# Performance work log

Hardware: AMD Instinct MI355X
Metric: run time of the kernel (lower is better)

Reference implementation:

```python
import jax, jax.numpy as jnp
import numpy as np

L, D, H, G, HS, I, V, B, T = 4, 1024, 16, 4, 64, 2816, 32000, 4, 512
THETA = 10000.0
EPS = 1e-6


def setup_inputs() -> dict:
    key = jax.random.key(0)
    ks = jax.random.split(key, 10)
    s = 0.02
    return {
        "input_ids": jax.random.randint(ks[0], (B, T), 0, V),
        "embed": jax.random.normal(ks[1], (V, D)) * s,      # tied with lm_head
        "q_w": jax.random.normal(ks[2], (L, D, D)) * s,     # torch Linear: [out, in]
        "q_b": jax.random.normal(ks[3], (L, D)) * s,
        "kv_w": jax.random.normal(ks[4], (L, 2 * G * HS, D)) * s,
        "kv_b": jax.random.normal(ks[5], (L, 2 * G * HS)) * s,
        "o_w": jax.random.normal(ks[6], (L, D, D)) * s,
        "ln1_w": jnp.ones((L, D)),
        "ln2_w": jnp.ones((L, D)),
        "gate_w": jax.random.normal(ks[7], (L, I, D)) * s,
        "up_w": jax.random.normal(ks[8], (L, I, D)) * s,
        "down_w": jax.random.normal(ks[9], (L, D, I)) * s,
        "last_w": jnp.ones((D,)),
    }


def rms_norm(x, w):
    return x * jax.lax.rsqrt(jnp.mean(x * x, axis=-1, keepdims=True) + EPS) * w


def rope_tables(t, hs):
    inv_freq = 1.0 / (THETA ** (jnp.arange(0, hs, 2, dtype=jnp.float32) / hs))
    ang = jnp.arange(t, dtype=jnp.float32)[:, None] * inv_freq[None, :]  # [T, hs/2]
    emb = jnp.concatenate([ang, ang], axis=-1)                           # [T, hs]
    return jnp.cos(emb), jnp.sin(emb)


def rotate_half(x):
    x1, x2 = jnp.split(x, 2, axis=-1)
    return jnp.concatenate([-x2, x1], axis=-1)


def reference(input_ids, embed, q_w, q_b, kv_w, kv_b, o_w, ln1_w, ln2_w, gate_w, up_w, down_w, last_w):
    x = embed[input_ids]  # [B, T, D]
    cos, sin = rope_tables(T, HS)                    # [T, HS] (buffers, const)
    c, s_ = cos[None, None], sin[None, None]         # [1, 1, T, HS]
    causal = jnp.tril(jnp.ones((T, T), dtype=bool))
    scale = 1.0 / np.sqrt(HS).astype(np.float32)
    for l in range(L):
        h = rms_norm(x, ln1_w[l])
        q = (h @ q_w[l].T + q_b[l]).reshape(B, T, H, HS).transpose(0, 2, 1, 3)  # bhtd
        kv = h @ kv_w[l].T + kv_b[l]
        k, v = jnp.split(kv, 2, axis=-1)
        k = k.reshape(B, T, G, HS).transpose(0, 2, 1, 3)  # bgtd
        v = v.reshape(B, T, G, HS).transpose(0, 2, 1, 3)
        k = jnp.repeat(k, H // G, axis=1)  # GQA kv repeat -> bhtd
        v = jnp.repeat(v, H // G, axis=1)
        q = q * c + rotate_half(q) * s_
        k = k * c + rotate_half(k) * s_
        attn = jnp.einsum('bhtd,bhsd->bhts', q, k) * scale
        attn = jnp.where(causal, attn, -jnp.inf)
        attn = jax.nn.softmax(attn, axis=-1)
        o = jnp.einsum('bhts,bhsd->bhtd', attn, v).transpose(0, 2, 1, 3).reshape(B, T, D)
        x = x + o @ o_w[l].T  # o_proj has no bias
        h = rms_norm(x, ln2_w[l])
        x = x + (jax.nn.silu(h @ gate_w[l].T) * (h @ up_w[l].T)) @ down_w[l].T  # SwiGLU
    x = rms_norm(x, last_w)
    return x @ embed.T  # tied lm_head -> logits [B, T, V]
```

## Files before the change

### kernel.cpp

```cpp
#include <hip/hip_runtime.h>
#include <hip/hip_bf16.h>
#include <stdint.h>


typedef __bf16 bf16x8 __attribute__((ext_vector_type(8)));
typedef __bf16 bf16x4 __attribute__((ext_vector_type(4)));
typedef float  f32x4  __attribute__((ext_vector_type(4)));

#define AS1 __attribute__((address_space(1)))
#define AS3 __attribute__((address_space(3)))

__device__ __forceinline__ void gld_lds16(const void* g, void* l) {
  __builtin_amdgcn_global_load_lds((const AS1 void*)g, (AS3 void*)l, 16, 0, 0);
}

__global__ __launch_bounds__(256) void cvt_kernel(const float* __restrict__ in,
                                                  __bf16* __restrict__ out, int n4) {
  for (int i = blockIdx.x * 256 + threadIdx.x; i < n4; i += gridDim.x * 256) {
    f32x4 v = __builtin_nontemporal_load(&((const f32x4*)in)[i]);
    bf16x4 o;
#pragma unroll
    for (int j = 0; j < 4; ++j) o[j] = (__bf16)v[j];
    ((bf16x4*)out)[i] = o;
  }
}

__global__ __launch_bounds__(256) void embed_kernel(const int* __restrict__ ids,
                                                    const float* __restrict__ emb,
                                                    float* __restrict__ x) {
  const int tok = blockIdx.x;
  const float* src = emb + (size_t)ids[tok] * 1024;
  float* dst = x + (size_t)tok * 1024;
#pragma unroll
  for (int j = 0; j < 4; ++j) {
    const int d = threadIdx.x + j * 256;
    dst[d] = src[d];
  }
}

__global__ __launch_bounds__(256) void rmsnorm_kernel(const float* __restrict__ x,
                                                      const float* __restrict__ wgt,
                                                      __bf16* __restrict__ out) {
  const int row = blockIdx.x;
  const float* xr = x + (size_t)row * 1024;
  float v[4];
  float ss = 0.f;
#pragma unroll
  for (int j = 0; j < 4; ++j) { v[j] = xr[threadIdx.x + j * 256]; ss += v[j] * v[j]; }
#pragma unroll
  for (int m = 1; m < 64; m <<= 1) ss += __shfl_xor(ss, m, 64);
  __shared__ float red[4];
  if ((threadIdx.x & 63) == 0) red[threadIdx.x >> 6] = ss;
  __syncthreads();
  const float tot = red[0] + red[1] + red[2] + red[3];
  const float sc = rsqrtf(tot * (1.f / 1024.f) + 1e-6f);
#pragma unroll
  for (int j = 0; j < 4; ++j) {
    const int d = threadIdx.x + j * 256;
    out[(size_t)row * 1024 + d] = (__bf16)(v[j] * sc * wgt[d]);
  }
}

#define GEMM_PREAMBLE                                              \
  const int t = threadIdx.x;                                       \
  const int lane = t & 63;                                         \
  const int w = t >> 6, wr = w >> 1, wc = w & 1;                   \
  const int lr = lane & 15;                                        \
  const int lk = (lane >> 4) * 8;                                  \
  const int sr = t >> 2;                                           \
  const int scol = (t & 3) * 8;

#define FLAT_SWZ(BMC, BNC)                                         \
  const int chunk_ = (int)(gridDim.x >> 3);                        \
  const int wg_ = (blockIdx.x & 7) * chunk_ + (blockIdx.x >> 3);   \
  const int bm = wg_ % (BMC);                                      \
  const int rest_ = wg_ / (BMC);                                   \
  const int bn = rest_ % (BNC);                                    \
  const int ks = rest_ / (BNC);                                    \
  (void)ks;

#define GEMM_FRAGS_MFMA                                            \
  bf16x8 af[4], bfr[4];                                            \
  _Pragma("unroll") for (int m = 0; m < 4; ++m)                    \
    af[m] = *(const bf16x8*)&As[(wr * 64 + m * 16 + lr) * 32 + lk];\
  _Pragma("unroll") for (int n = 0; n < 4; ++n)                    \
    bfr[n] = *(const bf16x8*)&Bs[(wc * 64 + n * 16 + lr) * 32 + lk];\
  _Pragma("unroll") for (int m = 0; m < 4; ++m)                    \
    _Pragma("unroll") for (int n = 0; n < 4; ++n)                  \
      acc[m][n] = __builtin_amdgcn_mfma_f32_16x16x32_bf16(af[m], bfr[n], acc[m][n], 0, 0, 0);

template <int EPI, int BMC, int BNC, int KSP>
__global__ __launch_bounds__(256) void gemm_bt(const __bf16* __restrict__ A,
                                               const __bf16* __restrict__ Bb,
                                               float* __restrict__ Cf,
                                               int K, int ldc) {
  __shared__ __bf16 As[128 * 32];
  __shared__ __bf16 Bs[128 * 32];
  GEMM_PREAMBLE
  FLAT_SWZ(BMC, BNC)
  const int klen = K / KSP;
  const int kbeg = ks * klen;

  const __bf16* a0 = A + (size_t)(bm * 128 + sr) * K + scol;
  const __bf16* a1 = A + (size_t)(bm * 128 + 64 + sr) * K + scol;
  const __bf16* bb0 = Bb + (size_t)(bn * 128 + sr) * K + scol;
  const __bf16* bb1 = Bb + (size_t)(bn * 128 + 64 + sr) * K + scol;

  f32x4 acc[4][4] = {};
  for (int k0 = kbeg; k0 < kbeg + klen; k0 += 32) {
    gld_lds16(a0 + k0, &As[t * 8]);
    gld_lds16(a1 + k0, &As[2048 + t * 8]);
    gld_lds16(bb0 + k0, &Bs[t * 8]);
    gld_lds16(bb1 + k0, &Bs[2048 + t * 8]);
    __syncthreads();
    GEMM_FRAGS_MFMA
    __syncthreads();
  }
  const int r0 = bm * 128 + wr * 64 + (lane >> 4) * 4;
  const int c0 = bn * 128 + wc * 64 + lr;
#pragma unroll
  for (int m = 0; m < 4; ++m)
#pragma unroll
    for (int r = 0; r < 4; ++r) {
      const size_t rowoff = (size_t)(r0 + m * 16 + r) * ldc;
#pragma unroll
      for (int n = 0; n < 4; ++n) {
        if (EPI == 3) Cf[rowoff + c0 + n * 16] = acc[m][n][r];
        else          atomicAdd(&Cf[rowoff + c0 + n * 16], acc[m][n][r]);
      }
    }
}

__global__ __launch_bounds__(256) void qkv_gemm(const __bf16* __restrict__ A,
                                                const __bf16* __restrict__ qw,
                                                const __bf16* __restrict__ kvw,
                                                const float* __restrict__ q_b,
                                                const float* __restrict__ kv_b,
                                                __bf16* __restrict__ qb,
                                                __bf16* __restrict__ kvb) {
  const int K = 1024;
  __shared__ __bf16 As[128 * 32];
  __shared__ __bf16 Bs[128 * 32];
  GEMM_PREAMBLE
  FLAT_SWZ(16, 12)
  const bool isq = bn < 8;
  const int bnn = isq ? bn : bn - 8;
  const __bf16* Bw = (isq ? qw : kvw) + (size_t)(bnn * 128) * K;

  const __bf16* a0 = A + (size_t)(bm * 128 + sr) * K + scol;
  const __bf16* a1 = A + (size_t)(bm * 128 + 64 + sr) * K + scol;
  const __bf16* bb0 = Bw + (size_t)sr * K + scol;
  const __bf16* bb1 = Bw + (size_t)(64 + sr) * K + scol;

  f32x4 acc[4][4] = {};
  for (int k0 = 0; k0 < K; k0 += 32) {
    gld_lds16(a0 + k0, &As[t * 8]);
    gld_lds16(a1 + k0, &As[2048 + t * 8]);
    gld_lds16(bb0 + k0, &Bs[t * 8]);
    gld_lds16(bb1 + k0, &Bs[2048 + t * 8]);
    __syncthreads();
    GEMM_FRAGS_MFMA
    __syncthreads();
  }

  const int ldc = isq ? 1024 : 512;
  __bf16* out = isq ? qb : kvb;
  const float* bias = isq ? q_b : kv_b;
  const int cb = bnn * 128 + wc * 64;
  const bool dorope = isq || (cb < 256);
  float bv[4];
#pragma unroll
  for (int n = 0; n < 4; ++n) bv[n] = bias[cb + n * 16 + lr];
  float inv0 = __expf((float)lr * -0.28782313662425574f);
  float inv1 = __expf((float)(16 + lr) * -0.28782313662425574f);

  const int r0 = bm * 128 + wr * 64 + (lane >> 4) * 4;
#pragma unroll
  for (int m = 0; m < 4; ++m)
#pragma unroll
    for (int r = 0; r < 4; ++r) {
      const int row = r0 + m * 16 + r;
      float c4[4];
#pragma unroll
      for (int n = 0; n < 4; ++n) c4[n] = acc[m][n][r] + bv[n];
      if (dorope) {
        const float pos = (float)(row & 511);
        float sg, cg;
        __sincosf(pos * inv0, &sg, &cg);
        float x1 = c4[0], x2 = c4[2];
        c4[0] = x1 * cg - x2 * sg;
        c4[2] = x2 * cg + x1 * sg;
        __sincosf(pos * inv1, &sg, &cg);
        x1 = c4[1]; x2 = c4[3];
        c4[1] = x1 * cg - x2 * sg;
        c4[3] = x2 * cg + x1 * sg;
      }
      const size_t rowoff = (size_t)row * ldc;
#pragma unroll
      for (int n = 0; n < 4; ++n) out[rowoff + cb + n * 16 + lr] = (__bf16)c4[n];
    }
}

__global__ __launch_bounds__(256) void gateup_gemm(const __bf16* __restrict__ A,
                                                   const __bf16* __restrict__ gw,
                                                   const __bf16* __restrict__ uw,
                                                   __bf16* __restrict__ gbuf,
                                                   __bf16* __restrict__ ubuf) {
  const int K = 1024;
  __shared__ __bf16 As[128 * 32];
  __shared__ __bf16 Bs[128 * 32];
  GEMM_PREAMBLE
  FLAT_SWZ(16, 44)
  const bool isg = bn < 22;
  const int bnn = isg ? bn : bn - 22;
  const __bf16* Bw = (isg ? gw : uw) + (size_t)(bnn * 128) * K;
  __bf16* out = isg ? gbuf : ubuf;

  const __bf16* a0 = A + (size_t)(bm * 128 + sr) * K + scol;
  const __bf16* a1 = A + (size_t)(bm * 128 + 64 + sr) * K + scol;
  const __bf16* bb0 = Bw + (size_t)sr * K + scol;
  const __bf16* bb1 = Bw + (size_t)(64 + sr) * K + scol;

  f32x4 acc[4][4] = {};
  for (int k0 = 0; k0 < K; k0 += 32) {
    gld_lds16(a0 + k0, &As[t * 8]);
    gld_lds16(a1 + k0, &As[2048 + t * 8]);
    gld_lds16(bb0 + k0, &Bs[t * 8]);
    gld_lds16(bb1 + k0, &Bs[2048 + t * 8]);
    __syncthreads();
    GEMM_FRAGS_MFMA
    __syncthreads();
  }
  const int r0 = bm * 128 + wr * 64 + (lane >> 4) * 4;
  const int c0 = bnn * 128 + wc * 64 + lr;
#pragma unroll
  for (int m = 0; m < 4; ++m)
#pragma unroll
    for (int r = 0; r < 4; ++r) {
      const size_t rowoff = (size_t)(r0 + m * 16 + r) * 2816;
#pragma unroll
      for (int n = 0; n < 4; ++n) out[rowoff + c0 + n * 16] = (__bf16)acc[m][n][r];
    }
}

__global__ __launch_bounds__(256) void down_gemm(const __bf16* __restrict__ g,
                                                 const __bf16* __restrict__ u,
                                                 const __bf16* __restrict__ Bb,
                                                 float* __restrict__ Cf) {
  const int K = 2816;
  __shared__ __bf16 As[128 * 32];
  __shared__ __bf16 Bs[128 * 32];
  GEMM_PREAMBLE
  FLAT_SWZ(16, 8)
  const int klen = 1408;
  const int kbeg = ks * klen;

  const size_t arow0 = (size_t)(bm * 128 + sr) * K + scol;
  const size_t arow1 = (size_t)(bm * 128 + 64 + sr) * K + scol;
  const __bf16* bb0 = Bb + (size_t)(bn * 128 + sr) * K + scol;
  const __bf16* bb1 = Bb + (size_t)(bn * 128 + 64 + sr) * K + scol;

  f32x4 acc[4][4] = {};
  for (int k0 = kbeg; k0 < kbeg + klen; k0 += 32) {
    {
      bf16x8 gv0 = *(const bf16x8*)(g + arow0 + k0);
      bf16x8 uv0 = *(const bf16x8*)(u + arow0 + k0);
      bf16x8 gv1 = *(const bf16x8*)(g + arow1 + k0);
      bf16x8 uv1 = *(const bf16x8*)(u + arow1 + k0);
      bf16x8 s0, s1;
#pragma unroll
      for (int j = 0; j < 8; ++j) {
        const float gf = (float)gv0[j];
        s0[j] = (__bf16)(gf / (1.f + __expf(-gf)) * (float)uv0[j]);
      }
#pragma unroll
      for (int j = 0; j < 8; ++j) {
        const float gf = (float)gv1[j];
        s1[j] = (__bf16)(gf / (1.f + __expf(-gf)) * (float)uv1[j]);
      }
      *(bf16x8*)&As[t * 8] = s0;
      *(bf16x8*)&As[2048 + t * 8] = s1;
    }
    gld_lds16(bb0 + k0, &Bs[t * 8]);
    gld_lds16(bb1 + k0, &Bs[2048 + t * 8]);
    __syncthreads();
    GEMM_FRAGS_MFMA
    __syncthreads();
  }
  const int r0 = bm * 128 + wr * 64 + (lane >> 4) * 4;
  const int c0 = bn * 128 + wc * 64 + lr;
#pragma unroll
  for (int m = 0; m < 4; ++m)
#pragma unroll
    for (int r = 0; r < 4; ++r) {
      const size_t rowoff = (size_t)(r0 + m * 16 + r) * 1024;
#pragma unroll
      for (int n = 0; n < 4; ++n) atomicAdd(&Cf[rowoff + c0 + n * 16], acc[m][n][r]);
    }
}

__global__ __launch_bounds__(512, 2) void lmhead_gemm(const __bf16* __restrict__ A,
                                                      const __bf16* __restrict__ Bb,
                                                      float* __restrict__ C) {
  __shared__ __bf16 lds[2][4][8192];
  const int t = threadIdx.x;
  const int lane = t & 63;
  const int w = t >> 6;
  const int wr = w >> 2;
  const int wc = w & 3;
  const int lr = lane & 15;
  const int lg = lane >> 4;
  const int sx = (lr & 7) << 4;

  const int wg = (blockIdx.x & 7) * 125 + (blockIdx.x >> 3);
  const int bm = wg & 7;
  const int bn = wg >> 3;

  int srow[2], scol[2];
#pragma unroll
  for (int j = 0; j < 2; ++j) {
    const int q = (t + j * 512) * 16;
    const int row = q >> 7;
    const int p = q ^ ((row & 7) << 4);
    srow[j] = row;
    scol[j] = (p & 127) >> 1;
  }

  auto STAGE = [&](int buf, int kt) {
#pragma unroll
    for (int ht = 0; ht < 4; ++ht) {
      const __bf16* base = (ht < 2)
          ? A + (size_t)(bm * 256 + ht * 128) * 1024
          : Bb + (size_t)(bn * 256 + (ht - 2) * 128) * 1024;
#pragma unroll
      for (int j = 0; j < 2; ++j) {
        gld_lds16(base + (size_t)srow[j] * 1024 + kt * 64 + scol[j],
                  (char*)&lds[buf][ht][0] + (size_t)(t + j * 512) * 16);
      }
    }
  };

  STAGE(0, 0);
  STAGE(1, 1);

  f32x4 acc[8][4] = {};
  for (int kt = 0; kt < 16; ++kt) {
    const int cur = kt & 1;
    if (kt < 15) asm volatile("s_waitcnt vmcnt(8)" ::: "memory");
    else         asm volatile("s_waitcnt vmcnt(0)" ::: "memory");
    __builtin_amdgcn_s_barrier();

    const char* Ab = (const char*)&lds[cur][wr][0];
    const char* Bbs = (const char*)&lds[cur][2 + (wc >> 1)][0];
    const int rB0 = (wc & 1) * 64;
#pragma unroll
    for (int ph = 0; ph < 4; ++ph) {
      const int m0 = (ph >> 1) * 4;
      const int n0 = (ph & 1) * 2;
      bf16x8 af[4][2], bfr[2][2];
#pragma unroll
      for (int mi = 0; mi < 4; ++mi)
#pragma unroll
        for (int ksl = 0; ksl < 2; ++ksl) {
          const int row = (m0 + mi) * 16 + lr;
          af[mi][ksl] = *(const bf16x8*)(Ab + ((row * 128 + ksl * 64 + lg * 16) ^ sx));
        }
#pragma unroll
      for (int ni = 0; ni < 2; ++ni)
#pragma unroll
        for (int ksl = 0; ksl < 2; ++ksl) {
          const int row = rB0 + (n0 + ni) * 16 + lr;
          bfr[ni][ksl] = *(const bf16x8*)(Bbs + ((row * 128 + ksl * 64 + lg * 16) ^ sx));
        }
      __builtin_amdgcn_s_setprio(1);
#pragma unroll
      for (int mi = 0; mi < 4; ++mi)
#pragma unroll
        for (int ni = 0; ni < 2; ++ni)
#pragma unroll
          for (int ksl = 0; ksl < 2; ++ksl)
            acc[m0 + mi][n0 + ni] = __builtin_amdgcn_mfma_f32_16x16x32_bf16(
                af[mi][ksl], bfr[ni][ksl], acc[m0 + mi][n0 + ni], 0, 0, 0);
      __builtin_amdgcn_s_setprio(0);
    }
    asm volatile("s_waitcnt lgkmcnt(0)" ::: "memory");
    __builtin_amdgcn_s_barrier();
    if (kt + 2 < 16) STAGE(cur, kt + 2);
  }

  const int r0 = bm * 256 + wr * 128 + lg * 4;
  const int c0 = bn * 256 + wc * 64 + lr;
#pragma unroll
  for (int m = 0; m < 8; ++m)
#pragma unroll
    for (int r = 0; r < 4; ++r) {
      float* crow = C + (size_t)(r0 + m * 16 + r) * 32000 + c0;
#pragma unroll
      for (int n = 0; n < 4; ++n)
        __builtin_nontemporal_store(acc[m][n][r], crow + n * 16);
    }
}

__global__ __launch_bounds__(256) void attn_kernel(const __bf16* __restrict__ q,
                                                   const __bf16* __restrict__ kv,
                                                   __bf16* __restrict__ o) {
  const int qt = blockIdx.x, hh = blockIdx.y, b = blockIdx.z;
  const int g = hh >> 2;
  const int t = threadIdx.x, lane = t & 63, w = t >> 6;
  const int lr = lane & 15, lg = lane >> 4;

  __shared__ __bf16 Vt[64 * 72];
  __shared__ __bf16 Ps[64 * 72];

  bf16x8 qa[2];
  {
    const size_t qoff = ((size_t)(b * 512 + qt * 64 + w * 16 + lr)) * 1024 + hh * 64;
    qa[0] = *(const bf16x8*)(q + qoff + lg * 8);
    qa[1] = *(const bf16x8*)(q + qoff + 32 + lg * 8);
  }

  f32x4 acc_o[4] = {};
  float mrow[4], lrow[4];
#pragma unroll
  for (int r = 0; r < 4; ++r) { mrow[r] = -1e30f; lrow[r] = 0.f; }

  const int srow = t >> 3;
  const int sdv = (t & 7) * 8;

  for (int kt = 0; kt <= qt; ++kt) {
    const size_t krow = ((size_t)(b * 512 + kt * 64 + srow)) * 512;
    {
      const __bf16* vsrc = kv + krow + 256 + g * 64 + sdv;
      bf16x8 v0 = *(const bf16x8*)vsrc;
      bf16x8 v1 = *(const bf16x8*)(vsrc + 32 * 512);
#pragma unroll
      for (int j = 0; j < 8; ++j) Vt[(sdv + j) * 72 + srow] = v0[j];
#pragma unroll
      for (int j = 0; j < 8; ++j) Vt[(sdv + j) * 72 + srow + 32] = v1[j];
    }
    __syncthreads();

    bf16x8 kb[4][2];
#pragma unroll
    for (int nf = 0; nf < 4; ++nf)
#pragma unroll
      for (int kc = 0; kc < 2; ++kc)
        kb[nf][kc] = *(const bf16x8*)(kv +
            ((size_t)(b * 512 + kt * 64 + nf * 16 + lr)) * 512 + g * 64 + kc * 32 + lg * 8);

    f32x4 s[4] = {};
#pragma unroll
    for (int nf = 0; nf < 4; ++nf)
#pragma unroll
      for (int kc = 0; kc < 2; ++kc)
        s[nf] = __builtin_amdgcn_mfma_f32_16x16x32_bf16(qa[kc], kb[nf][kc], s[nf], 0, 0, 0);

    float pm[4][4], mx[4];
    const int qg = qt * 64 + w * 16 + lg * 4;
    const int kg = kt * 64 + lr;
#pragma unroll
    for (int r = 0; r < 4; ++r) mx[r] = -1e30f;
#pragma unroll
    for (int nf = 0; nf < 4; ++nf)
#pragma unroll
      for (int r = 0; r < 4; ++r) {
        float vv = s[nf][r] * 0.125f;
        vv = (kg + nf * 16 <= qg + r) ? vv : -1e30f;
        pm[nf][r] = vv;
        mx[r] = fmaxf(mx[r], vv);
      }
#pragma unroll
    for (int msk = 1; msk < 16; msk <<= 1)
#pragma unroll
      for (int r = 0; r < 4; ++r) mx[r] = fmaxf(mx[r], __shfl_xor(mx[r], msk, 64));

    float rs[4];
#pragma unroll
    for (int r = 0; r < 4; ++r) {
      const float mn = fmaxf(mrow[r], mx[r]);
      const float f = __expf(mrow[r] - mn);
      mrow[r] = mn;
      lrow[r] *= f;
#pragma unroll
      for (int df = 0; df < 4; ++df) acc_o[df][r] *= f;
      float rsum = 0.f;
#pragma unroll
      for (int nf = 0; nf < 4; ++nf) {
        const float pp = __expf(pm[nf][r] - mn);
        pm[nf][r] = pp;
        rsum += pp;
      }
      rs[r] = rsum;
    }
#pragma unroll
    for (int msk = 1; msk < 16; msk <<= 1)
#pragma unroll
      for (int r = 0; r < 4; ++r) rs[r] += __shfl_xor(rs[r], msk, 64);
#pragma unroll
    for (int r = 0; r < 4; ++r) lrow[r] += rs[r];

#pragma unroll
    for (int nf = 0; nf < 4; ++nf)
#pragma unroll
      for (int r = 0; r < 4; ++r)
        Ps[(w * 16 + lg * 4 + r) * 72 + nf * 16 + lr] = (__bf16)pm[nf][r];

#pragma unroll
    for (int df = 0; df < 4; ++df)
#pragma unroll
      for (int kc = 0; kc < 2; ++kc) {
        bf16x8 pa = *(const bf16x8*)&Ps[(w * 16 + lr) * 72 + kc * 32 + lg * 8];
        bf16x8 vb = *(const bf16x8*)&Vt[(df * 16 + lr) * 72 + kc * 32 + lg * 8];
        acc_o[df] = __builtin_amdgcn_mfma_f32_16x16x32_bf16(pa, vb, acc_o[df], 0, 0, 0);
      }
    __syncthreads();
  }

#pragma unroll
  for (int df = 0; df < 4; ++df)
#pragma unroll
    for (int r = 0; r < 4; ++r) {
      const int trow = qt * 64 + w * 16 + lg * 4 + r;
      o[((size_t)(b * 512 + trow)) * 1024 + hh * 64 + df * 16 + lr] =
          (__bf16)(acc_o[df][r] / lrow[r]);
    }
}

extern "C" void kernel_launch(void* const* d_in, const int* in_sizes, int n_in,
                              void* d_out, int out_size, void* d_ws, size_t ws_size,
                              hipStream_t stream) {
  const int* ids = (const int*)d_in[0];
  const float* emb_f = (const float*)d_in[1];
  const float* qw_f = (const float*)d_in[2];
  const float* q_b = (const float*)d_in[3];
  const float* kvw_f = (const float*)d_in[4];
  const float* kv_b = (const float*)d_in[5];
  const float* ow_f = (const float*)d_in[6];
  const float* ln1 = (const float*)d_in[7];
  const float* ln2 = (const float*)d_in[8];
  const float* gw_f = (const float*)d_in[9];
  const float* uw_f = (const float*)d_in[10];
  const float* dw_f = (const float*)d_in[11];
  const float* lw = (const float*)d_in[12];
  float* out = (float*)d_out;

  char* p = (char*)d_ws;
  float* x = (float*)p;        p += (size_t)2048 * 1024 * 4;
  __bf16* h = (__bf16*)p;      p += (size_t)2048 * 1024 * 2;
  __bf16* qb = (__bf16*)p;     p += (size_t)2048 * 1024 * 2;
  __bf16* kvb = (__bf16*)p;    p += (size_t)2048 * 512 * 2;
  __bf16* ao = (__bf16*)p;     p += (size_t)2048 * 1024 * 2;
  __bf16* gb = (__bf16*)p;     p += (size_t)2048 * 2816 * 2;
  __bf16* ub = (__bf16*)p;     p += (size_t)2048 * 2816 * 2;
  __bf16* emb_b = (__bf16*)p;  p += (size_t)32000 * 1024 * 2;
  __bf16* qw_b = (__bf16*)p;   p += (size_t)4 * 1024 * 1024 * 2;
  __bf16* kvw_b = (__bf16*)p;  p += (size_t)4 * 512 * 1024 * 2;
  __bf16* ow_b = (__bf16*)p;   p += (size_t)4 * 1024 * 1024 * 2;
  __bf16* gw_b = (__bf16*)p;   p += (size_t)4 * 2816 * 1024 * 2;
  __bf16* uw_b = (__bf16*)p;   p += (size_t)4 * 2816 * 1024 * 2;
  __bf16* dw_b = (__bf16*)p;   p += (size_t)4 * 2816 * 1024 * 2;

  cvt_kernel<<<2048, 256, 0, stream>>>(emb_f, emb_b, 32000 * 1024 / 4);
  cvt_kernel<<<1024, 256, 0, stream>>>(qw_f, qw_b, 4 * 1024 * 1024 / 4);
  cvt_kernel<<<1024, 256, 0, stream>>>(kvw_f, kvw_b, 4 * 512 * 1024 / 4);
  cvt_kernel<<<1024, 256, 0, stream>>>(ow_f, ow_b, 4 * 1024 * 1024 / 4);
  cvt_kernel<<<1024, 256, 0, stream>>>(gw_f, gw_b, 4 * 2816 * 1024 / 4);
  cvt_kernel<<<1024, 256, 0, stream>>>(uw_f, uw_b, 4 * 2816 * 1024 / 4);
  cvt_kernel<<<1024, 256, 0, stream>>>(dw_f, dw_b, 4 * 2816 * 1024 / 4);

  embed_kernel<<<2048, 256, 0, stream>>>(ids, emb_f, x);
  for (int l = 0; l < 4; ++l) {
    rmsnorm_kernel<<<2048, 256, 0, stream>>>(x, ln1 + l * 1024, h);
    qkv_gemm<<<192, 256, 0, stream>>>(
        h, qw_b + (size_t)l * 1024 * 1024, kvw_b + (size_t)l * 512 * 1024,
        q_b + l * 1024, kv_b + l * 512, qb, kvb);
    attn_kernel<<<dim3(8, 16, 4), 256, 0, stream>>>(qb, kvb, ao);
    gemm_bt<4, 16, 8, 2><<<256, 256, 0, stream>>>(
        ao, ow_b + (size_t)l * 1024 * 1024, x, 1024, 1024);
    rmsnorm_kernel<<<2048, 256, 0, stream>>>(x, ln2 + l * 1024, h);
    gateup_gemm<<<704, 256, 0, stream>>>(
        h, gw_b + (size_t)l * 2816 * 1024, uw_b + (size_t)l * 2816 * 1024, gb, ub);
    down_gemm<<<256, 256, 0, stream>>>(
        gb, ub, dw_b + (size_t)l * 1024 * 2816, x);
  }
  rmsnorm_kernel<<<2048, 256, 0, stream>>>(x, lw, h);
  lmhead_gemm<<<1000, 512, 0, stream>>>(h, emb_b, out);
}
```

Before: 1.064 ms.

## Generalize 256x256 GEMM with finer-grained pipelining and reuse it for gate/up projection

```diff
diff --git a/kernel.cpp b/kernel.cpp
--- a/kernel.cpp
+++ b/kernel.cpp
@@ -201,50 +201,7 @@
     }
 }
 
-__global__ __launch_bounds__(256) void gateup_gemm(const __bf16* __restrict__ A,
-                                                   const __bf16* __restrict__ gw,
-                                                   const __bf16* __restrict__ uw,
-                                                   __bf16* __restrict__ gbuf,
-                                                   __bf16* __restrict__ ubuf) {
-  const int K = 1024;
-  __shared__ __bf16 As[128 * 32];
-  __shared__ __bf16 Bs[128 * 32];
-  GEMM_PREAMBLE
-  FLAT_SWZ(16, 44)
-  const bool isg = bn < 22;
-  const int bnn = isg ? bn : bn - 22;
-  const __bf16* Bw = (isg ? gw : uw) + (size_t)(bnn * 128) * K;
-  __bf16* out = isg ? gbuf : ubuf;
-
-  const __bf16* a0 = A + (size_t)(bm * 128 + sr) * K + scol;
-  const __bf16* a1 = A + (size_t)(bm * 128 + 64 + sr) * K + scol;
-  const __bf16* bb0 = Bw + (size_t)sr * K + scol;
-  const __bf16* bb1 = Bw + (size_t)(64 + sr) * K + scol;
-
-  f32x4 acc[4][4] = {};
-  for (int k0 = 0; k0 < K; k0 += 32) {
-    gld_lds16(a0 + k0, &As[t * 8]);
-    gld_lds16(a1 + k0, &As[2048 + t * 8]);
-    gld_lds16(bb0 + k0, &Bs[t * 8]);
-    gld_lds16(bb1 + k0, &Bs[2048 + t * 8]);
-    __syncthreads();
-    GEMM_FRAGS_MFMA
-    __syncthreads();
-  }
-  const int r0 = bm * 128 + wr * 64 + (lane >> 4) * 4;
-  const int c0 = bnn * 128 + wc * 64 + lr;
-#pragma unroll
-  for (int m = 0; m < 4; ++m)
-#pragma unroll
-    for (int r = 0; r < 4; ++r) {
-      const size_t rowoff = (size_t)(r0 + m * 16 + r) * 2816;
-#pragma unroll
-      for (int n = 0; n < 4; ++n) out[rowoff + c0 + n * 16] = (__bf16)acc[m][n][r];
-    }
-}
-
-__global__ __launch_bounds__(256) void down_gemm(const __bf16* __restrict__ g,
-                                                 const __bf16* __restrict__ u,
+__global__ __launch_bounds__(256) void down_gemm(const __bf16* __restrict__ gu,
                                                  const __bf16* __restrict__ Bb,
                                                  float* __restrict__ Cf) {
   const int K = 2816;
@@ -255,18 +212,18 @@
   const int klen = 1408;
   const int kbeg = ks * klen;
 
-  const size_t arow0 = (size_t)(bm * 128 + sr) * K + scol;
-  const size_t arow1 = (size_t)(bm * 128 + 64 + sr) * K + scol;
+  const size_t arow0 = (size_t)(bm * 128 + sr) * 5632 + scol;
+  const size_t arow1 = (size_t)(bm * 128 + 64 + sr) * 5632 + scol;
   const __bf16* bb0 = Bb + (size_t)(bn * 128 + sr) * K + scol;
   const __bf16* bb1 = Bb + (size_t)(bn * 128 + 64 + sr) * K + scol;
 
   f32x4 acc[4][4] = {};
   for (int k0 = kbeg; k0 < kbeg + klen; k0 += 32) {
     {
-      bf16x8 gv0 = *(const bf16x8*)(g + arow0 + k0);
-      bf16x8 uv0 = *(const bf16x8*)(u + arow0 + k0);
-      bf16x8 gv1 = *(const bf16x8*)(g + arow1 + k0);
-      bf16x8 uv1 = *(const bf16x8*)(u + arow1 + k0);
+      bf16x8 gv0 = *(const bf16x8*)(gu + arow0 + k0);
+      bf16x8 uv0 = *(const bf16x8*)(gu + arow0 + 2816 + k0);
+      bf16x8 gv1 = *(const bf16x8*)(gu + arow1 + k0);
+      bf16x8 uv1 = *(const bf16x8*)(gu + arow1 + 2816 + k0);
       bf16x8 s0, s1;
 #pragma unroll
       for (int j = 0; j < 8; ++j) {
@@ -299,9 +256,19 @@
     }
 }
 
-__global__ __launch_bounds__(512, 2) void lmhead_gemm(const __bf16* __restrict__ A,
-                                                      const __bf16* __restrict__ Bb,
-                                                      float* __restrict__ C) {
+#define SYNC_MFMA(MH, NH, BR)                                      \
+  __builtin_amdgcn_s_barrier();                                    \
+  asm volatile("s_waitcnt lgkmcnt(0)" ::: "memory");               \
+  __builtin_amdgcn_sched_barrier(0);                               \
+  MFMA16(MH, NH, BR);                                              \
+  __builtin_amdgcn_s_barrier();
+
+template <int EPI>
+__global__ __launch_bounds__(512, 2) void gemm256(const __bf16* __restrict__ A,
+                                                  const __bf16* __restrict__ Bb,
+                                                  float* __restrict__ Cf,
+                                                  __bf16* __restrict__ Cb,
+                                                  int ldc) {
   __shared__ __bf16 lds[2][4][8192];
   const int t = threadIdx.x;
   const int lane = t & 63;
@@ -312,7 +279,8 @@
   const int lg = lane >> 4;
   const int sx = (lr & 7) << 4;
 
-  const int wg = (blockIdx.x & 7) * 125 + (blockIdx.x >> 3);
+  const int chunk = (int)gridDim.x >> 3;
+  const int wg = ((int)blockIdx.x & 7) * chunk + ((int)blockIdx.x >> 3);
   const int bm = wg & 7;
   const int bn = wg >> 3;
 
@@ -326,66 +294,90 @@
     scol[j] = (p & 127) >> 1;
   }
 
-  auto STAGE = [&](int buf, int kt) {
-#pragma unroll
-    for (int ht = 0; ht < 4; ++ht) {
-      const __bf16* base = (ht < 2)
-          ? A + (size_t)(bm * 256 + ht * 128) * 1024
-          : Bb + (size_t)(bn * 256 + (ht - 2) * 128) * 1024;
-#pragma unroll
-      for (int j = 0; j < 2; ++j) {
-        gld_lds16(base + (size_t)srow[j] * 1024 + kt * 64 + scol[j],
-                  (char*)&lds[buf][ht][0] + (size_t)(t + j * 512) * 16);
-      }
-    }
+  auto STAGE1 = [&](int buf, int ht, int kt) {
+    const __bf16* base = (ht < 2) ? A + (size_t)(bm * 256 + ht * 128) * 1024
+                                  : Bb + (size_t)(bn * 256 + (ht - 2) * 128) * 1024;
+#pragma unroll
+    for (int j = 0; j < 2; ++j)
+      gld_lds16(base + (size_t)srow[j] * 1024 + kt * 64 + scol[j],
+                (char*)&lds[buf][ht][0] + (size_t)(t + j * 512) * 16);
   };
 
-  STAGE(0, 0);
-  STAGE(1, 1);
-
+  bf16x8 afr[4][2], b0r[2][2], b1r[2][2];
   f32x4 acc[8][4] = {};
-  for (int kt = 0; kt < 16; ++kt) {
-    const int cur = kt & 1;
-    if (kt < 15) asm volatile("s_waitcnt vmcnt(8)" ::: "memory");
-    else         asm volatile("s_waitcnt vmcnt(0)" ::: "memory");
-    __builtin_amdgcn_s_barrier();
-
-    const char* Ab = (const char*)&lds[cur][wr][0];
-    const char* Bbs = (const char*)&lds[cur][2 + (wc >> 1)][0];
-    const int rB0 = (wc & 1) * 64;
-#pragma unroll
-    for (int ph = 0; ph < 4; ++ph) {
-      const int m0 = (ph >> 1) * 4;
-      const int n0 = (ph & 1) * 2;
-      bf16x8 af[4][2], bfr[2][2];
-#pragma unroll
-      for (int mi = 0; mi < 4; ++mi)
-#pragma unroll
-        for (int ksl = 0; ksl < 2; ++ksl) {
-          const int row = (m0 + mi) * 16 + lr;
-          af[mi][ksl] = *(const bf16x8*)(Ab + ((row * 128 + ksl * 64 + lg * 16) ^ sx));
-        }
+
+  auto LDA = [&](int buf, int mh) {
+    const char* Ab = (const char*)&lds[buf][wr][0];
+#pragma unroll
+    for (int mi = 0; mi < 4; ++mi)
+#pragma unroll
+      for (int ksl = 0; ksl < 2; ++ksl) {
+        const int row = (mh * 4 + mi) * 16 + lr;
+        afr[mi][ksl] = *(const bf16x8*)(Ab + ((row * 128 + ksl * 64 + lg * 16) ^ sx));
+      }
+  };
+  auto LDB = [&](int buf, int nh, bf16x8 (&br)[2][2]) {
+    const char* Bs = (const char*)&lds[buf][2 + (wc >> 1)][0];
+    const int rB0 = (wc & 1) * 64 + nh * 32;
+#pragma unroll
+    for (int ni = 0; ni < 2; ++ni)
+#pragma unroll
+      for (int ksl = 0; ksl < 2; ++ksl) {
+        const int row = rB0 + ni * 16 + lr;
+        br[ni][ksl] = *(const bf16x8*)(Bs + ((row * 128 + ksl * 64 + lg * 16) ^ sx));
+      }
+  };
+  auto MFMA16 = [&](int mh, int nh, bf16x8 (&br)[2][2]) {
+    __builtin_amdgcn_s_setprio(1);
+#pragma unroll
+    for (int mi = 0; mi < 4; ++mi)
 #pragma unroll
       for (int ni = 0; ni < 2; ++ni)
 #pragma unroll
-        for (int ksl = 0; ksl < 2; ++ksl) {
-          const int row = rB0 + (n0 + ni) * 16 + lr;
-          bfr[ni][ksl] = *(const bf16x8*)(Bbs + ((row * 128 + ksl * 64 + lg * 16) ^ sx));
-        }
-      __builtin_amdgcn_s_setprio(1);
-#pragma unroll
-      for (int mi = 0; mi < 4; ++mi)
-#pragma unroll
-        for (int ni = 0; ni < 2; ++ni)
-#pragma unroll
-          for (int ksl = 0; ksl < 2; ++ksl)
-            acc[m0 + mi][n0 + ni] = __builtin_amdgcn_mfma_f32_16x16x32_bf16(
-                af[mi][ksl], bfr[ni][ksl], acc[m0 + mi][n0 + ni], 0, 0, 0);
-      __builtin_amdgcn_s_setprio(0);
-    }
-    asm volatile("s_waitcnt lgkmcnt(0)" ::: "memory");
-    __builtin_amdgcn_s_barrier();
-    if (kt + 2 < 16) STAGE(cur, kt + 2);
+        for (int ksl = 0; ksl < 2; ++ksl)
+          acc[mh * 4 + mi][nh * 2 + ni] = __builtin_amdgcn_mfma_f32_16x16x32_bf16(
+              afr[mi][ksl], br[ni][ksl], acc[mh * 4 + mi][nh * 2 + ni], 0, 0, 0);
+    __builtin_amdgcn_s_setprio(0);
+  };
+
+  STAGE1(0, 2, 0); STAGE1(0, 0, 0); STAGE1(0, 3, 0); STAGE1(0, 1, 0);
+  STAGE1(1, 2, 1); STAGE1(1, 0, 1);
+  asm volatile("s_waitcnt vmcnt(4)" ::: "memory");
+  __builtin_amdgcn_s_barrier();
+
+  for (int j = 0; j < 8; ++j) {
+    const int T1 = 2 * j + 1;
+    const bool pf = (j < 7);
+    LDA(0, 0); LDB(0, 0, b0r);
+    STAGE1(1, 3, T1);
+    SYNC_MFMA(0, 0, b0r)
+    LDB(0, 1, b1r);
+    STAGE1(1, 1, T1);
+    SYNC_MFMA(0, 1, b1r)
+    LDA(0, 1);
+    if (pf) STAGE1(0, 2, T1 + 1);
+    SYNC_MFMA(1, 1, b1r)
+    if (pf) {
+      STAGE1(0, 0, T1 + 1);
+      asm volatile("s_waitcnt vmcnt(4)" ::: "memory");
+    } else {
+      asm volatile("s_waitcnt vmcnt(0)" ::: "memory");
+    }
+    SYNC_MFMA(1, 0, b0r)
+    LDA(1, 0); LDB(1, 0, b0r);
+    if (pf) STAGE1(0, 3, T1 + 1);
+    SYNC_MFMA(0, 0, b0r)
+    LDB(1, 1, b1r);
+    if (pf) STAGE1(0, 1, T1 + 1);
+    SYNC_MFMA(0, 1, b1r)
+    LDA(1, 1);
+    if (pf) STAGE1(1, 2, T1 + 2);
+    SYNC_MFMA(1, 1, b1r)
+    if (pf) {
+      STAGE1(1, 0, T1 + 2);
+      asm volatile("s_waitcnt vmcnt(4)" ::: "memory");
+    }
+    SYNC_MFMA(1, 0, b0r)
   }
 
   const int r0 = bm * 256 + wr * 128 + lg * 4;
@@ -394,10 +386,16 @@
   for (int m = 0; m < 8; ++m)
 #pragma unroll
     for (int r = 0; r < 4; ++r) {
-      float* crow = C + (size_t)(r0 + m * 16 + r) * 32000 + c0;
-#pragma unroll
-      for (int n = 0; n < 4; ++n)
-        __builtin_nontemporal_store(acc[m][n][r], crow + n * 16);
+      if (EPI == 0) {
+        float* crow = Cf + (size_t)(r0 + m * 16 + r) * ldc + c0;
+#pragma unroll
+        for (int n = 0; n < 4; ++n)
+          __builtin_nontemporal_store(acc[m][n][r], crow + n * 16);
+      } else {
+        __bf16* crow = Cb + (size_t)(r0 + m * 16 + r) * ldc + c0;
+#pragma unroll
+        for (int n = 0; n < 4; ++n) crow[n * 16] = (__bf16)acc[m][n][r];
+      }
     }
 }
 
@@ -550,22 +548,25 @@
   __bf16* qb = (__bf16*)p;     p += (size_t)2048 * 1024 * 2;
   __bf16* kvb = (__bf16*)p;    p += (size_t)2048 * 512 * 2;
   __bf16* ao = (__bf16*)p;     p += (size_t)2048 * 1024 * 2;
-  __bf16* gb = (__bf16*)p;     p += (size_t)2048 * 2816 * 2;
-  __bf16* ub = (__bf16*)p;     p += (size_t)2048 * 2816 * 2;
+  __bf16* guB = (__bf16*)p;    p += (size_t)2048 * 5632 * 2;
   __bf16* emb_b = (__bf16*)p;  p += (size_t)32000 * 1024 * 2;
   __bf16* qw_b = (__bf16*)p;   p += (size_t)4 * 1024 * 1024 * 2;
   __bf16* kvw_b = (__bf16*)p;  p += (size_t)4 * 512 * 1024 * 2;
   __bf16* ow_b = (__bf16*)p;   p += (size_t)4 * 1024 * 1024 * 2;
-  __bf16* gw_b = (__bf16*)p;   p += (size_t)4 * 2816 * 1024 * 2;
-  __bf16* uw_b = (__bf16*)p;   p += (size_t)4 * 2816 * 1024 * 2;
+  __bf16* guw_b = (__bf16*)p;  p += (size_t)4 * 5632 * 1024 * 2;
   __bf16* dw_b = (__bf16*)p;   p += (size_t)4 * 2816 * 1024 * 2;
 
   cvt_kernel<<<2048, 256, 0, stream>>>(emb_f, emb_b, 32000 * 1024 / 4);
   cvt_kernel<<<1024, 256, 0, stream>>>(qw_f, qw_b, 4 * 1024 * 1024 / 4);
   cvt_kernel<<<1024, 256, 0, stream>>>(kvw_f, kvw_b, 4 * 512 * 1024 / 4);
   cvt_kernel<<<1024, 256, 0, stream>>>(ow_f, ow_b, 4 * 1024 * 1024 / 4);
-  cvt_kernel<<<1024, 256, 0, stream>>>(gw_f, gw_b, 4 * 2816 * 1024 / 4);
-  cvt_kernel<<<1024, 256, 0, stream>>>(uw_f, uw_b, 4 * 2816 * 1024 / 4);
+  for (int l = 0; l < 4; ++l) {
+    cvt_kernel<<<1024, 256, 0, stream>>>(gw_f + (size_t)l * 2816 * 1024,
+                                         guw_b + (size_t)l * 5632 * 1024, 2816 * 1024 / 4);
+    cvt_kernel<<<1024, 256, 0, stream>>>(uw_f + (size_t)l * 2816 * 1024,
+                                         guw_b + (size_t)l * 5632 * 1024 + (size_t)2816 * 1024,
+                                         2816 * 1024 / 4);
+  }
   cvt_kernel<<<1024, 256, 0, stream>>>(dw_f, dw_b, 4 * 2816 * 1024 / 4);
 
   embed_kernel<<<2048, 256, 0, stream>>>(ids, emb_f, x);
@@ -578,11 +579,11 @@
     gemm_bt<4, 16, 8, 2><<<256, 256, 0, stream>>>(
         ao, ow_b + (size_t)l * 1024 * 1024, x, 1024, 1024);
     rmsnorm_kernel<<<2048, 256, 0, stream>>>(x, ln2 + l * 1024, h);
-    gateup_gemm<<<704, 256, 0, stream>>>(
-        h, gw_b + (size_t)l * 2816 * 1024, uw_b + (size_t)l * 2816 * 1024, gb, ub);
+    gemm256<1><<<176, 512, 0, stream>>>(
+        h, guw_b + (size_t)l * 5632 * 1024, nullptr, guB, 5632);
     down_gemm<<<256, 256, 0, stream>>>(
-        gb, ub, dw_b + (size_t)l * 1024 * 2816, x);
+        guB, dw_b + (size_t)l * 1024 * 2816, x);
   }
   rmsnorm_kernel<<<2048, 256, 0, stream>>>(x, lw, h);
-  lmhead_gemm<<<1000, 512, 0, stream>>>(h, emb_b, out);
-}
+  gemm256<0><<<1000, 512, 0, stream>>>(h, emb_b, out, nullptr, 32000);
+}
```

Result: no change. 1.069 ms (+0.5%).
